# Performance work log

Measured on AMD Instinct MI355X. Metric: run time of the kernel, lower is better.

Reference implementation:

```python
import jax, jax.numpy as jnp
import numpy as np

B, N, E = 2, 2048, 1024
H = 16
NE = 16                                  # num experts
TOPN = 2
CAP = max(4, int(N * 1.25 / NE))         # expert capacity = 160 (train, cf=1.25)
HFF = int(E * 4 * 2 / 3)                 # 2730, Expert_alt hidden
EPS = 1e-9
BLOCK = 64                               # spatial block size for block-causal mask


def setup_inputs():
    key = jax.random.key(0)
    ks = jax.random.split(key, 16)
    def nrm(k, shape, s=0.02):
        return jax.random.normal(k, shape, dtype=jnp.float32) * s
    # block-causal mask (tril over time blocks, repeat_interleave spatially); True = masked
    blk = np.tril(np.ones((N // BLOCK, N // BLOCK)))
    blk = np.repeat(np.repeat(blk, BLOCK, axis=0), BLOCK, axis=1)
    attn_mask = jnp.asarray(~blk.astype(bool))
    return dict(
        x=jax.random.normal(ks[0], (B, N, E), jnp.float32),
        attn_mask=attn_mask,
        in_proj_w=nrm(ks[1], (3 * E, E)),
        in_proj_b=jnp.zeros((3 * E,), jnp.float32),
        out_proj_w=nrm(ks[2], (E, E)),
        out_proj_b=jnp.zeros((E,), jnp.float32),
        rms_gamma=jnp.ones((E,), jnp.float32),
        gate_w=nrm(ks[3], (NE, E)),
        ln_g=jnp.ones((NE, E), jnp.float32),
        ln_b=jnp.zeros((NE, E), jnp.float32),
        w1=nrm(ks[4], (NE, HFF, E)),
        b1=jnp.zeros((NE, HFF), jnp.float32),
        w2=nrm(ks[5], (NE, E, HFF)),
        b2=jnp.zeros((NE, E), jnp.float32),
        route_unif=jax.random.uniform(ks[6], (TOPN, B, N), jnp.float32),
    )


def _layernorm(t, g, b, eps=1e-5):
    mu = t.mean(-1, keepdims=True)
    var = ((t - mu) ** 2).mean(-1, keepdims=True)
    return (t - mu) * jax.lax.rsqrt(var + eps) * g + b


def _forward(x, attn_mask, in_proj_w, in_proj_b, out_proj_w, out_proj_b,
             rms_gamma, gate_w, ln_g, ln_b, w1, b1, w2, b2, route_unif):
    dh = E // H
    # ---- multi-head self-attention (torch nn.MultiheadAttention math) ----
    qkv = x @ in_proj_w.T + in_proj_b                       # (B,N,3E)
    q, k, v = jnp.split(qkv, 3, axis=-1)
    to_heads = lambda t: t.reshape(B, N, H, dh).transpose(0, 2, 1, 3)
    q, k, v = to_heads(q), to_heads(k), to_heads(v)
    scores = jnp.einsum('bhqd,bhkd->bhqk', q, k) / jnp.sqrt(jnp.float32(dh))
    scores = jnp.where(attn_mask[None, None], -jnp.inf, scores)
    attn = jax.nn.softmax(scores, axis=-1)
    o = jnp.einsum('bhqk,bhkd->bhqd', attn, v).transpose(0, 2, 1, 3).reshape(B, N, E)
    o = o @ out_proj_w.T + out_proj_b
    y = o + x                                               # residual around MHA

    # ---- SparseMoEBlock: RMSNorm prenorm -> MoE -> residual ----
    residual = y
    nrm = y / jnp.clip(jnp.linalg.norm(y, axis=-1, keepdims=True), 1e-12)
    moe_in = nrm * jnp.sqrt(jnp.float32(E)) * rms_gamma

    # ---- top-2 gating (st-moe TopNGating, training mode) ----
    logits = moe_in @ gate_w.T                              # (B,N,NE)
    raw_gates = jax.nn.softmax(logits, axis=-1)
    gates_v, gate_idx = jax.lax.top_k(raw_gates, TOPN)      # (B,N,2)
    gates = jnp.moveaxis(gates_v, -1, 0)                    # (2,B,N)
    gate_idx = jnp.moveaxis(gate_idx, -1, 0)
    one_hot_idx = jax.nn.one_hot(gate_idx, NE, dtype=jnp.float32)  # (2,B,N,NE)
    mask = one_hot_idx
    mask_1 = mask[0]
    denom = jnp.clip(gates.sum(0, keepdims=True), EPS)
    gates = gates / denom
    threshold = jnp.array([EPS, 0.2], jnp.float32)[:, None, None]
    should_route = route_unif < gates / jnp.clip(threshold, EPS)
    should_route = should_route.at[0].set(True)             # always route to top-1
    mask = mask * should_route[..., None].astype(jnp.float32)
    mask_cumsum = jnp.cumsum(mask, axis=-2) - mask          # exclusive cumsum over N

    positions, masks_k = [], []
    prev = jnp.zeros((B, 1, NE), jnp.float32)
    capf = jnp.float32(CAP)
    for n_ in range(TOPN):
        pos = (mask_cumsum[n_] + prev) * mask[n_]           # (B,N,NE)
        mk = mask[n_] * (pos < capf).astype(jnp.float32)    # drop over-capacity
        prev = prev + mk.sum(axis=-2, keepdims=True)
        positions.append(pos.sum(-1))                       # (B,N)
        masks_k.append(mk)
    positions = jnp.stack(positions)                        # (2,B,N)
    mask = jnp.stack(masks_k)
    mask_flat = mask.sum(-1)                                # (2,B,N)
    gates = gates * mask_flat

    pos_oh = jax.nn.one_hot(positions.astype(jnp.int32), CAP, dtype=jnp.float32)  # (2,B,N,CAP)
    combine = jnp.einsum('kbn,kbn,kbne,kbnc->bnec', gates, mask_flat, one_hot_idx, pos_oh)
    dispatch_hard = (combine > 0).astype(jnp.float32)
    dispatch = dispatch_hard + combine - jax.lax.stop_gradient(combine)  # straight-through

    # ---- aux losses ----
    density_1 = mask_1.mean(-2)                             # (B,NE)
    density_proxy = raw_gates.mean(-2)
    balance_loss = (density_proxy * density_1).mean() * jnp.float32(NE ** 2)
    router_z_loss = jnp.mean(jax.nn.logsumexp(logits, axis=-1) ** 2)

    # ---- dispatch -> experts -> combine ----
    expert_inputs = jnp.einsum('bnd,bnec->ebcd', moe_in, dispatch)  # (NE,B,CAP,E)

    def expert_fn(g, bl, W1, B1, W2, B2, xin):
        h = _layernorm(xin, g, bl)
        h = h @ W1.T + B1
        h = jnp.where(h >= 0, h, 0.01 * h)                  # LeakyReLU(0.01)
        return h @ W2.T + B2

    expert_out = jax.vmap(expert_fn)(ln_g, ln_b, w1, b1, w2, b2, expert_inputs)
    moe_out = jnp.einsum('bnec,ebcd->bnd', combine, expert_out)

    out = moe_out + residual
    total_aux = balance_loss * 0.01 + router_z_loss * 0.001
    return out, total_aux, balance_loss, router_z_loss


def reference(x, attn_mask, in_proj_w, in_proj_b, out_proj_w, out_proj_b,
              rms_gamma, gate_w, ln_g, ln_b, w1, b1, w2, b2, route_unif):
    return _forward(x, attn_mask, in_proj_w, in_proj_b, out_proj_w, out_proj_b,
                    rms_gamma, gate_w, ln_g, ln_b, w1, b1, w2, b2, route_unif)
```

## Files before the change

### kernel.cpp

```cpp
#include <hip/hip_runtime.h>
#include <hip/hip_bf16.h>
#include <cstdint>

#define NSEQ  2048
#define BSZ   2
#define NTOK  4096
#define EDIM  1024
#define NEXP  16
#define CAPC  160
#define HFF_R 2730
#define HFF_P 2752

typedef __bf16 bf16_t;
typedef __bf16 bf16x8 __attribute__((ext_vector_type(8)));
typedef __bf16 bf16x4 __attribute__((ext_vector_type(4)));
typedef float  f32x4  __attribute__((ext_vector_type(4)));
typedef unsigned int uint32;

__device__ inline bf16x8 zero8() {
    bf16x8 v;
#pragma unroll
    for (int i = 0; i < 8; i++) v[i] = (bf16_t)0.f;
    return v;
}
__device__ inline bf16x8 pack8(float4 a, float4 b) {
    bf16x8 v;
    v[0]=(bf16_t)a.x; v[1]=(bf16_t)a.y; v[2]=(bf16_t)a.z; v[3]=(bf16_t)a.w;
    v[4]=(bf16_t)b.x; v[5]=(bf16_t)b.y; v[6]=(bf16_t)b.z; v[7]=(bf16_t)b.w;
    return v;
}
struct hl_t { bf16_t h, l; };
__device__ inline hl_t split1(float f) {
    hl_t r;
    r.h = (bf16_t)f;
    r.l = (bf16_t)(f - (float)r.h);
    return r;
}

template <int EPI, int C_SPLIT>
__global__ __launch_bounds__(256) void gemm_split(
    const float* __restrict__ A, const float* __restrict__ Bw,
    const float* __restrict__ bias, const float* __restrict__ resid,
    bf16_t* __restrict__ Chi, bf16_t* __restrict__ Clo, float* __restrict__ Cf,
    int M, int N, int K, int scale_cut, float scale_val)
// ... 72 lines not shown
                acc[i][j] = __builtin_amdgcn_mfma_f32_16x16x32_bf16(amh[i], bnl[j], acc[i][j], 0, 0, 0);
                acc[i][j] = __builtin_amdgcn_mfma_f32_16x16x32_bf16(aml[i], bnh[j], acc[i][j], 0, 0, 0);
            }
        __builtin_amdgcn_s_setprio(0);
        __syncthreads();
    }

#pragma unroll
    for (int i = 0; i < 4; i++) {
        int mgb = m0 + wm * 64 + i * 16 + lg * 4;
#pragma unroll
        for (int j = 0; j < 4; j++) {
            int ng = n0 + wn * 64 + j * 16 + l15;
            float bval = bias[ng];
#pragma unroll
            for (int r = 0; r < 4; r++) {
                int mg = mgb + r;
                float val = acc[i][j][r] + bval;
                if (scale_cut > 0 && ng < scale_cut) val *= scale_val;
                if (EPI == 2) val += resid[(long)mg * N + ng];
                long idx = (long)mg * N + ng;
                if (C_SPLIT) {
                    bf16_t hi = (bf16_t)val;
                    Chi[idx] = hi;
                    Clo[idx] = (bf16_t)(val - (float)hi);
                } else {
                    Cf[idx] = val;
                }
            }
        }
    }
}

template <int EPI, int C_BF16>
__global__ __launch_bounds__(256) void gemm_nt64(
    const bf16_t* __restrict__ Av, const float* __restrict__ Bw,
    const float* __restrict__ bias, void* __restrict__ Cv,
    int M, int N, int Nwr, int KA, int KB,
    long sAe, long sBe, long sBiasE, long sCe, int ldc)
{
    __shared__ __align__(16) bf16_t Alds[64 * 72];
    __shared__ __align__(16) bf16_t Blds[64 * 72];
    const int t = threadIdx.x;
    const int e = blockIdx.z;
    const int m0 = blockIdx.y * 64, n0 = blockIdx.x * 64;
    const int lane = t & 63, l15 = lane & 15, lg = lane >> 4;
    const int wid = t >> 6, wm = wid >> 1, wn = wid & 1;
    const int srow = t >> 2, scol = (t & 3) * 16;

    f32x4 acc[2][2];
    const f32x4 zf = {0.f, 0.f, 0.f, 0.f};
#pragma unroll
    for (int i = 0; i < 2; i++)
#pragma unroll
        for (int j = 0; j < 2; j++) acc[i][j] = zf;

    bf16x8 sa0, sa1;
    float4 sb0, sb1, sb2, sb3;
    const float4 zf4 = {0.f, 0.f, 0.f, 0.f};
    auto LOADA = [&](int k0) {
        int mg = m0 + srow;
        sa0 = zero8(); sa1 = zero8();
        if (mg < M) {
            const bf16_t* ap = Av + (long)e * sAe + (long)mg * KA + k0 + scol;
            sa0 = *(const bf16x8*)ap;
            sa1 = *(const bf16x8*)(ap + 8);
        }
    };
    auto LOADB = [&](int k0) {
        int ng = n0 + srow;
        if (ng < N) {
            const float* bp = Bw + (long)e * sBe + (long)ng * KB + k0 + scol;
            if (k0 + 64 <= KB) {
                sb0 = *(const float4*)bp;       sb1 = *(const float4*)(bp + 4);
                sb2 = *(const float4*)(bp + 8); sb3 = *(const float4*)(bp + 12);
            } else {
                float v[16];
#pragma unroll
                for (int i = 0; i < 16; i++) {
                    int kk = k0 + scol + i;
                    v[i] = (kk < KB) ? bp[i] : 0.f;
                }
                sb0 = *(float4*)&v[0];  sb1 = *(float4*)&v[4];
                sb2 = *(float4*)&v[8];  sb3 = *(float4*)&v[12];
            }
        } else {
            sb0 = zf4; sb1 = zf4; sb2 = zf4; sb3 = zf4;
        }
    };
    auto WRITEAB = [&]() {
        *(bf16x8*)&Alds[srow * 72 + scol]     = sa0;
        *(bf16x8*)&Alds[srow * 72 + scol + 8] = sa1;
        *(bf16x8*)&Blds[srow * 72 + scol]     = pack8(sb0, sb1);
        *(bf16x8*)&Blds[srow * 72 + scol + 8] = pack8(sb2, sb3);
    };

    LOADA(0); LOADB(0);
    for (int k0 = 0; k0 < KA; k0 += 64) {
        WRITEAB();
        __syncthreads();
        if (k0 + 64 < KA) { LOADA(k0 + 64); LOADB(k0 + 64); }
#pragma unroll
        for (int ks = 0; ks < 2; ks++) {
            bf16x8 am[2], bn[2];
#pragma unroll
            for (int i = 0; i < 2; i++)
                am[i] = *(const bf16x8*)&Alds[(wm * 32 + i * 16 + l15) * 72 + ks * 32 + lg * 8];
#pragma unroll
            for (int j = 0; j < 2; j++)
                bn[j] = *(const bf16x8*)&Blds[(wn * 32 + j * 16 + l15) * 72 + ks * 32 + lg * 8];
            __builtin_amdgcn_s_setprio(1);
#pragma unroll
            for (int i = 0; i < 2; i++)
#pragma unroll
                for (int j = 0; j < 2; j++)
                    acc[i][j] = __builtin_amdgcn_mfma_f32_16x16x32_bf16(am[i], bn[j], acc[i][j], 0, 0, 0);
            __builtin_amdgcn_s_setprio(0);
        }
        __syncthreads();
    }

    const float* biasp = bias + (long)e * sBiasE;
#pragma unroll
    for (int i = 0; i < 2; i++) {
        int mgb = m0 + wm * 32 + i * 16 + lg * 4;
#pragma unroll
        for (int j = 0; j < 2; j++) {
            int ng = n0 + wn * 32 + j * 16 + l15;
            if (ng < Nwr) {
                float bval = (ng < N) ? biasp[ng] : 0.f;
#pragma unroll
                for (int r = 0; r < 4; r++) {
                    int mg = mgb + r;
                    if (mg < M) {
                        float val = acc[i][j][r] + bval;
                        if (EPI == 1) val = (val >= 0.f) ? val : 0.01f * val;
                        if (ng >= N) val = 0.f;
                        long cidx = (long)e * sCe + (long)mg * ldc + ng;
                        if (C_BF16) ((bf16_t*)Cv)[cidx] = (bf16_t)val;
                        else        ((float*)Cv)[cidx] = val;
                    }
                }
            }
        }
    }
}

__global__ __launch_bounds__(256) void attn_split(const bf16_t* __restrict__ qh,
                                                  const bf16_t* __restrict__ ql,
                                                  float* __restrict__ o)
{
    __shared__ __align__(16) bf16_t KhS[64 * 72], KlS[64 * 72];
    __shared__ __align__(16) bf16_t VhS[64 * 72], VlS[64 * 72];
    __shared__ __align__(16) bf16_t PhS[4][2][16 * 72], PlS[4][2][16 * 72];

    const int id = blockIdx.x;
    const int x  = id & 7;
    const int s  = id >> 3;
    const int b  = s >> 5;
    const int s5 = s & 31;
    const int qraw = s5 & 15;
    const int h  = x + 8 * (s5 >> 4);
    const int qt = b ? (15 - qraw) : qraw;
    const int nkb = 2 * qt + 2;

    const int t = threadIdx.x, wid = t >> 6, lane = t & 63, l15 = lane & 15, lg = lane >> 4;
    const int krow = t >> 2, kdc = (t & 3) * 16;
    const int vk = t & 63, vdg = (t >> 6) * 16;
    const long kvb = (long)(b * NSEQ) * 3072 + 1024 + h * 64;
    const f32x4 zf = {0.f, 0.f, 0.f, 0.f};

    const long qo0 = (long)(b * NSEQ + qt * 128 + wid * 16 + l15) * 3072 + h * 64 + lg * 8;
    const long qo1 = qo0 + (long)64 * 3072;
    bf16x8 q0h0 = *(const bf16x8*)(qh + qo0), q0h1 = *(const bf16x8*)(qh + qo0 + 32);
    bf16x8 q0l0 = *(const bf16x8*)(ql + qo0), q0l1 = *(const bf16x8*)(ql + qo0 + 32);
    bf16x8 q1h0 = *(const bf16x8*)(qh + qo1), q1h1 = *(const bf16x8*)(qh + qo1 + 32);
    bf16x8 q1l0 = *(const bf16x8*)(ql + qo1), q1l1 = *(const bf16x8*)(ql + qo1 + 32);

    f32x4 O0[4], O1[4];
    float m0r[4], l0r[4], m1r[4], l1r[4];
#pragma unroll
    for (int r = 0; r < 4; r++) {
        O0[r] = zf; O1[r] = zf;
        m0r[r] = -1e30f; l0r[r] = 0.f; m1r[r] = -1e30f; l1r[r] = 0.f;
    }

    bf16x8 skh0, skh1, skl0, skl1, svh0, svh1, svl0, svl1;
    auto LOADKV = [&](int kb) {
        long ko = kvb + (long)(kb * 64 + krow) * 3072 + kdc;
        skh0 = *(const bf16x8*)(qh + ko); skh1 = *(const bf16x8*)(qh + ko + 8);
        skl0 = *(const bf16x8*)(ql + ko); skl1 = *(const bf16x8*)(ql + ko + 8);
        long vo = kvb + 1024 + (long)(kb * 64 + vk) * 3072 + vdg;
        svh0 = *(const bf16x8*)(qh + vo); svh1 = *(const bf16x8*)(qh + vo + 8);
        svl0 = *(const bf16x8*)(ql + vo); svl1 = *(const bf16x8*)(ql + vo + 8);
    };
    auto WRITEKV = [&]() {
        *(bf16x8*)&KhS[krow * 72 + kdc]     = skh0;
        *(bf16x8*)&KhS[krow * 72 + kdc + 8] = skh1;
        *(bf16x8*)&KlS[krow * 72 + kdc]     = skl0;
        *(bf16x8*)&KlS[krow * 72 + kdc + 8] = skl1;
#pragma unroll
        for (int i = 0; i < 8; i++) {
            VhS[(vdg + i) * 72 + vk]     = svh0[i];
            VhS[(vdg + 8 + i) * 72 + vk] = svh1[i];
            VlS[(vdg + i) * 72 + vk]     = svl0[i];
            VlS[(vdg + 8 + i) * 72 + vk] = svl1[i];
        }
    };

    LOADKV(0);
    for (int kb = 0; kb < nkb; kb++) {
        __syncthreads();
        WRITEKV();
        __syncthreads();
        if (kb + 1 < nkb) LOADKV(kb + 1);
        const bool g0a = (kb < nkb - 1);
        f32x4 s0[4], s1[4];
        __builtin_amdgcn_s_setprio(1);
#pragma unroll
        for (int ks = 0; ks < 4; ks++) {
            int base = (ks * 16 + l15) * 72 + lg * 8;
            bf16x8 kh0 = *(const bf16x8*)&KhS[base];
            bf16x8 kh1 = *(const bf16x8*)&KhS[base + 32];
            bf16x8 kl0 = *(const bf16x8*)&KlS[base];
            bf16x8 kl1 = *(const bf16x8*)&KlS[base + 32];
            f32x4 a = zf;
            a = __builtin_amdgcn_mfma_f32_16x16x32_bf16(q1h0, kh0, a, 0, 0, 0);
            a = __builtin_amdgcn_mfma_f32_16x16x32_bf16(q1h1, kh1, a, 0, 0, 0);
            a = __builtin_amdgcn_mfma_f32_16x16x32_bf16(q1h0, kl0, a, 0, 0, 0);
            a = __builtin_amdgcn_mfma_f32_16x16x32_bf16(q1h1, kl1, a, 0, 0, 0);
            a = __builtin_amdgcn_mfma_f32_16x16x32_bf16(q1l0, kh0, a, 0, 0, 0);
            a = __builtin_amdgcn_mfma_f32_16x16x32_bf16(q1l1, kh1, a, 0, 0, 0);
            s1[ks] = a;
            f32x4 c = zf;
            if (g0a) {
                c = __builtin_amdgcn_mfma_f32_16x16x32_bf16(q0h0, kh0, c, 0, 0, 0);
                c = __builtin_amdgcn_mfma_f32_16x16x32_bf16(q0h1, kh1, c, 0, 0, 0);
                c = __builtin_amdgcn_mfma_f32_16x16x32_bf16(q0h0, kl0, c, 0, 0, 0);
                c = __builtin_amdgcn_mfma_f32_16x16x32_bf16(q0h1, kl1, c, 0, 0, 0);
                c = __builtin_amdgcn_mfma_f32_16x16x32_bf16(q0l0, kh0, c, 0, 0, 0);
                c = __builtin_amdgcn_mfma_f32_16x16x32_bf16(q0l1, kh1, c, 0, 0, 0);
            }
            s0[ks] = c;
        }
        __builtin_amdgcn_s_setprio(0);
        {
            float alpha[4];
#pragma unroll
            for (int r = 0; r < 4; r++) {
                float mt = fmaxf(fmaxf(s1[0][r], s1[1][r]), fmaxf(s1[2][r], s1[3][r]));
#pragma unroll
                for (int m = 1; m < 16; m <<= 1) mt = fmaxf(mt, __shfl_xor(mt, m));
                float mn = fmaxf(m1r[r], mt);
                alpha[r] = __expf(m1r[r] - mn);
                m1r[r] = mn;
            }
            float ladd[4] = {0.f, 0.f, 0.f, 0.f};
#pragma unroll
            for (int ks = 0; ks < 4; ks++)
#pragma unroll
                for (int r = 0; r < 4; r++) {
                    float p = __expf(s1[ks][r] - m1r[r]);
                    s1[ks][r] = p;
                    ladd[r] += p;
                }
#pragma unroll
            for (int r = 0; r < 4; r++) {
#pragma unroll
                for (int m = 1; m < 16; m <<= 1) ladd[r] += __shfl_xor(ladd[r], m);
                l1r[r] = l1r[r] * alpha[r] + ladd[r];
            }
#pragma unroll
            for (int sb = 0; sb < 4; sb++)
#pragma unroll
                for (int r = 0; r < 4; r++) O1[sb][r] *= alpha[r];
            bf16_t* pwh = &PhS[wid][1][0];
            bf16_t* pwl = &PlS[wid][1][0];
#pragma unroll
            for (int ks = 0; ks < 4; ks++)
#pragma unroll
                for (int r = 0; r < 4; r++) {
                    hl_t pv = split1(s1[ks][r]);
                    pwh[(lg * 4 + r) * 72 + ks * 16 + l15] = pv.h;
                    pwl[(lg * 4 + r) * 72 + ks * 16 + l15] = pv.l;
                }
        }
        if (g0a) {
            float alpha[4];
#pragma unroll
            for (int r = 0; r < 4; r++) {
                float mt = fmaxf(fmaxf(s0[0][r], s0[1][r]), fmaxf(s0[2][r], s0[3][r]));
#pragma unroll
                for (int m = 1; m < 16; m <<= 1) mt = fmaxf(mt, __shfl_xor(mt, m));
                float mn = fmaxf(m0r[r], mt);
                alpha[r] = __expf(m0r[r] - mn);
                m0r[r] = mn;
            }
            float ladd[4] = {0.f, 0.f, 0.f, 0.f};
#pragma unroll
            for (int ks = 0; ks < 4; ks++)
#pragma unroll
                for (int r = 0; r < 4; r++) {
                    float p = __expf(s0[ks][r] - m0r[r]);
                    s0[ks][r] = p;
                    ladd[r] += p;
                }
#pragma unroll
            for (int r = 0; r < 4; r++) {
#pragma unroll
                for (int m = 1; m < 16; m <<= 1) ladd[r] += __shfl_xor(ladd[r], m);
                l0r[r] = l0r[r] * alpha[r] + ladd[r];
            }
#pragma unroll
            for (int sb = 0; sb < 4; sb++)
#pragma unroll
                for (int r = 0; r < 4; r++) O0[sb][r] *= alpha[r];
            bf16_t* pwh = &PhS[wid][0][0];
            bf16_t* pwl = &PlS[wid][0][0];
#pragma unroll
            for (int ks = 0; ks < 4; ks++)
#pragma unroll
                for (int r = 0; r < 4; r++) {
                    hl_t pv = split1(s0[ks][r]);
                    pwh[(lg * 4 + r) * 72 + ks * 16 + l15] = pv.h;
                    pwl[(lg * 4 + r) * 72 + ks * 16 + l15] = pv.l;
                }
        }
        __builtin_amdgcn_s_setprio(1);
#pragma unroll
        for (int kst = 0; kst < 2; kst++) {
            bf16x8 pf1h = *(const bf16x8*)&PhS[wid][1][l15 * 72 + kst * 32 + lg * 8];
            bf16x8 pf1l = *(const bf16x8*)&PlS[wid][1][l15 * 72 + kst * 32 + lg * 8];
            bf16x8 pf0h, pf0l;
            if (g0a) {
                pf0h = *(const bf16x8*)&PhS[wid][0][l15 * 72 + kst * 32 + lg * 8];
                pf0l = *(const bf16x8*)&PlS[wid][0][l15 * 72 + kst * 32 + lg * 8];
            }
#pragma unroll
            for (int sb = 0; sb < 4; sb++) {
                int base = (sb * 16 + l15) * 72 + kst * 32 + lg * 8;
                bf16x8 vfh = *(const bf16x8*)&VhS[base];
                bf16x8 vfl = *(const bf16x8*)&VlS[base];
                O1[sb] = __builtin_amdgcn_mfma_f32_16x16x32_bf16(pf1h, vfh, O1[sb], 0, 0, 0);
                O1[sb] = __builtin_amdgcn_mfma_f32_16x16x32_bf16(pf1h, vfl, O1[sb], 0, 0, 0);
                O1[sb] = __builtin_amdgcn_mfma_f32_16x16x32_bf16(pf1l, vfh, O1[sb], 0, 0, 0);
                if (g0a) {
                    O0[sb] = __builtin_amdgcn_mfma_f32_16x16x32_bf16(pf0h, vfh, O0[sb], 0, 0, 0);
                    O0[sb] = __builtin_amdgcn_mfma_f32_16x16x32_bf16(pf0h, vfl, O0[sb], 0, 0, 0);
                    O0[sb] = __builtin_amdgcn_mfma_f32_16x16x32_bf16(pf0l, vfh, O0[sb], 0, 0, 0);
                }
            }
        }
        __builtin_amdgcn_s_setprio(0);
    }
#pragma unroll
    for (int sb = 0; sb < 4; sb++)
#pragma unroll
        for (int r = 0; r < 4; r++) {
            int qg0 = qt * 128 + wid * 16 + lg * 4 + r;
            int col = h * 64 + sb * 16 + l15;
            o[(long)(b * NSEQ + qg0) * 1024 + col] = O0[sb][r] / l0r[r];
            o[(long)(b * NSEQ + qg0 + 64) * 1024 + col] = O1[sb][r] / l1r[r];
        }
}

__global__ __launch_bounds__(256) void rmsnorm_kernel(const float* __restrict__ y,
                                                      const float* __restrict__ gamma,
                                                      float* __restrict__ moe)
{
    long base = (long)blockIdx.x * 1024;
    float4 v = ((const float4*)(y + base))[threadIdx.x];
    float ss = v.x * v.x + v.y * v.y + v.z * v.z + v.w * v.w;
#pragma unroll
    for (int m = 32; m; m >>= 1) ss += __shfl_xor(ss, m);
    __shared__ float ls[4];
    if ((threadIdx.x & 63) == 0) ls[threadIdx.x >> 6] = ss;
    __syncthreads();
    float tot = ls[0] + ls[1] + ls[2] + ls[3];
    float sc = 32.0f / fmaxf(sqrtf(tot), 1e-12f);
    float4 g = ((const float4*)gamma)[threadIdx.x];
    float4 ov;
    ov.x = v.x * sc * g.x; ov.y = v.y * sc * g.y; ov.z = v.z * sc * g.z; ov.w = v.w * sc * g.w;
    ((float4*)(moe + base))[threadIdx.x] = ov;
}

__global__ __launch_bounds__(256) void gating_kernel(
    const float* __restrict__ moe, const float* __restrict__ gw,
    const float* __restrict__ runif, uint32* __restrict__ tokpack,
    float* __restrict__ tokg, float* __restrict__ acc)
{
    const int wid = threadIdx.x >> 6, lane = threadIdx.x & 63;
    const int tk = blockIdx.x * 4 + wid;
    const int b = tk >> 11, n = tk & 2047;
    float xv[16];
    const float4* xr4 = (const float4*)(moe + (long)tk * 1024 + lane * 16);
#pragma unroll
// ... 246 lines not shown
    const float* out_w = (const float*)d_in[4];
    const float* out_b = (const float*)d_in[5];
    const float* rg    = (const float*)d_in[6];
    const float* gw    = (const float*)d_in[7];
    const float* lng   = (const float*)d_in[8];
    const float* lnb   = (const float*)d_in[9];
    const float* w1    = (const float*)d_in[10];
    const float* b1    = (const float*)d_in[11];
    const float* w2    = (const float*)d_in[12];
    const float* b2    = (const float*)d_in[13];
    const float* runif = (const float*)d_in[14];
    float* out = (float*)d_out;

    size_t off = 0;
    char* wsb = (char*)d_ws;
    auto take = [&](size_t bytes) -> char* {
        char* p = wsb + off;
        off += (bytes + 255) & ~(size_t)255;
        return p;
    };
    bf16_t* qkvh = (bf16_t*)take((size_t)NTOK * 3072 * 2);
    bf16_t* qkvl = (bf16_t*)take((size_t)NTOK * 3072 * 2);
    float*  obuf = (float*)take((size_t)NTOK * 1024 * 4);
    float*  ybuf = (float*)take((size_t)NTOK * 1024 * 4);
    float*  moe  = (float*)take((size_t)NTOK * 1024 * 4);
    bf16_t* eln  = (bf16_t*)take((size_t)NEXP * BSZ * CAPC * 1024 * 2);
    bf16_t* hbuf = (bf16_t*)take((size_t)NEXP * BSZ * CAPC * HFF_P * 2);
    uint32* tokpack = (uint32*)take(NTOK * 4);
    float*  tokg = (float*)take(NTOK * 8);
    uint32* r0   = (uint32*)take(NTOK * 4);
    uint32* r1   = (uint32*)take(NTOK * 4);
    int*    prev = (int*)take(128);
    float*  acc  = (float*)take(1024);
    float*  ein  = (float*)qkvl;
    float*  eoutv = (float*)qkvh;

    zero_acc_kernel<<<1, 128, 0, stream>>>(acc);

    gemm_split<0, 1><<<dim3(24, 32), 256, 0, stream>>>(
        x, in_w, in_b, nullptr, qkvh, qkvl, nullptr,
        NTOK, 3072, 1024, 1024, 0.125f);

    attn_split<<<dim3(512), 256, 0, stream>>>(qkvh, qkvl, obuf);

    gemm_split<2, 0><<<dim3(8, 32), 256, 0, stream>>>(
        obuf, out_w, out_b, x, nullptr, nullptr, ybuf,
        NTOK, 1024, 1024, 0, 1.0f);

    rmsnorm_kernel<<<NTOK, 256, 0, stream>>>(ybuf, rg, moe);
    gating_kernel<<<NTOK / 4, 256, 0, stream>>>(moe, gw, runif, tokpack, tokg, acc);
    scan_kernel<<<dim3(BSZ), 512, 0, stream>>>(tokpack, r0, r1, prev);
    gather_kernel<<<NTOK, 256, 0, stream>>>(moe, r0, r1, prev, ein);
    expert_ln_kernel<<<NEXP * BSZ * CAPC, 256, 0, stream>>>(ein, lng, lnb, eln);

    gemm_nt64<1, 1><<<dim3(43, 5, 16), 256, 0, stream>>>(
        eln, w1, b1, hbuf, 320, HFF_R, HFF_P, 1024, 1024,
        (long)320 * 1024, (long)HFF_R * 1024, HFF_R, (long)320 * HFF_P, HFF_P);

    gemm_nt64<0, 0><<<dim3(16, 5, 16), 256, 0, stream>>>(
        hbuf, w2, b2, eoutv, 320, 1024, 1024, HFF_P, HFF_R,
        (long)320 * HFF_P, (long)1024 * HFF_R, 1024, (long)320 * 1024, 1024);

    combine_kernel<<<NTOK, 256, 0, stream>>>(ybuf, eoutv, r0, r1, tokg, prev, out);
    finalize_kernel<<<1, 64, 0, stream>>>(acc, out + (size_t)NTOK * 1024);
}
```

Baseline: 687.9 us.

## Split attention KV range across blocks with merge kernel; widen expert GEMM1 tiles

Attention now gives each block one short and one long query tile (pairing pr with 15-pr), and splits the KV range of each into two halves handled by separate blocks. Each block writes unnormalized partial outputs plus per-row max and sum, and a new merge kernel combines the two halves with log-sum-exp weights. The aim is to even out causal load imbalance across blocks. Separately, the first expert GEMM switches to a new 64x128 tile kernel with K step 32, which halves the grid in N and increases reuse of each A tile. The cost is extra fp32 partial-output traffic, an added launch for the merge, and reuse of the eln buffer as scratch.

```diff
diff --git a/kernel.cpp b/kernel.cpp
--- a/kernel.cpp
+++ b/kernel.cpp
@@ -10,6 +10,7 @@
 #define CAPC  160
 #define HFF_R 2730
 #define HFF_P 2752
+#define OTOT  4194304
 
 typedef __bf16 bf16_t;
 typedef __bf16 bf16x8 __attribute__((ext_vector_type(8)));
@@ -148,6 +149,121 @@
     }
 }
 
+template <int EPI, int C_BF16, int BM>
+__global__ __launch_bounds__(256) void gemm_ntA(
+    const bf16_t* __restrict__ Av, const float* __restrict__ Bw,
+    const float* __restrict__ bias, void* __restrict__ Cv,
+    int M, int N, int Nwr, int KA, int KB,
+    long sAe, long sBe, long sBiasE, long sCe, int ldc)
+{
+    constexpr int MI = BM / 32;
+    __shared__ __align__(16) bf16_t Alds[BM * 40];
+    __shared__ __align__(16) bf16_t Blds[128 * 40];
+    const int t = threadIdx.x;
+    const int e = blockIdx.z;
+    const int m0 = blockIdx.y * BM, n0 = blockIdx.x * 128;
+    const int lane = t & 63, l15 = lane & 15, lg = lane >> 4;
+    const int wid = t >> 6, wm = wid >> 1, wn = wid & 1;
+    const int arow = (BM == 128) ? (t >> 1) : (t >> 2);
+    const int acol = (BM == 128) ? ((t & 1) * 16) : ((t & 3) * 8);
+    const int brow = t >> 1, bcol = (t & 1) * 16;
+
+    f32x4 acc[MI][4];
+    const f32x4 zf = {0.f, 0.f, 0.f, 0.f};
+#pragma unroll
+    for (int i = 0; i < MI; i++)
+#pragma unroll
+        for (int j = 0; j < 4; j++) acc[i][j] = zf;
+
+    bf16x8 sa0, sa1;
+    float4 sb0, sb1, sb2, sb3;
+    const float4 zf4 = {0.f, 0.f, 0.f, 0.f};
+    auto LOADA = [&](int k0) {
+        int mg = m0 + arow;
+        sa0 = zero8();
+        if (BM == 128) sa1 = zero8();
+        if (mg < M) {
+            const bf16_t* ap = Av + (long)e * sAe + (long)mg * KA + k0 + acol;
+            sa0 = *(const bf16x8*)ap;
+            if (BM == 128) sa1 = *(const bf16x8*)(ap + 8);
+        }
+    };
+    auto LOADB = [&](int k0) {
+        int ng = n0 + brow;
+        if (ng < N) {
+            const float* bp = Bw + (long)e * sBe + (long)ng * KB + k0 + bcol;
+            if (k0 + 32 <= KB) {
+                sb0 = *(const float4*)bp;       sb1 = *(const float4*)(bp + 4);
+                sb2 = *(const float4*)(bp + 8); sb3 = *(const float4*)(bp + 12);
+            } else {
+                float v[16];
+#pragma unroll
+                for (int i = 0; i < 16; i++) {
+                    int kk = k0 + bcol + i;
+                    v[i] = (kk < KB) ? bp[i] : 0.f;
+                }
+                sb0 = *(float4*)&v[0];  sb1 = *(float4*)&v[4];
+                sb2 = *(float4*)&v[8];  sb3 = *(float4*)&v[12];
+            }
+        } else {
+            sb0 = zf4; sb1 = zf4; sb2 = zf4; sb3 = zf4;
+        }
+    };
+    auto WRITEAB = [&]() {
+        *(bf16x8*)&Alds[arow * 40 + acol] = sa0;
+        if (BM == 128) *(bf16x8*)&Alds[arow * 40 + acol + 8] = sa1;
+        *(bf16x8*)&Blds[brow * 40 + bcol] = pack8(sb0, sb1);
+        *(bf16x8*)&Blds[brow * 40 + bcol + 8] = pack8(sb2, sb3);
+    };
+
+    LOADA(0); LOADB(0);
+    for (int k0 = 0; k0 < KA; k0 += 32) {
+        WRITEAB();
+        __syncthreads();
+        if (k0 + 32 < KA) { LOADA(k0 + 32); LOADB(k0 + 32); }
+        bf16x8 am[MI], bn[4];
+#pragma unroll
+        for (int i = 0; i < MI; i++)
+            am[i] = *(const bf16x8*)&Alds[(wm * (BM / 2) + i * 16 + l15) * 40 + lg * 8];
+#pragma unroll
+        for (int j = 0; j < 4; j++)
+            bn[j] = *(const bf16x8*)&Blds[(wn * 64 + j * 16 + l15) * 40 + lg * 8];
+        __builtin_amdgcn_s_setprio(1);
+#pragma unroll
+        for (int i = 0; i < MI; i++)
+#pragma unroll
+            for (int j = 0; j < 4; j++)
+                acc[i][j] = __builtin_amdgcn_mfma_f32_16x16x32_bf16(am[i], bn[j], acc[i][j], 0, 0, 0);
+        __builtin_amdgcn_s_setprio(0);
+        __syncthreads();
+    }
+
+    const float* biasp = bias + (long)e * sBiasE;
+#pragma unroll
+    for (int i = 0; i < MI; i++) {
+        int mgb = m0 + wm * (BM / 2) + i * 16 + lg * 4;
+#pragma unroll
+        for (int j = 0; j < 4; j++) {
+            int ng = n0 + wn * 64 + j * 16 + l15;
+            if (ng < Nwr) {
+                float bval = (ng < N) ? biasp[ng] : 0.f;
+#pragma unroll
+                for (int r = 0; r < 4; r++) {
+                    int mg = mgb + r;
+                    if (mg < M) {
+                        float val = acc[i][j][r] + bval;
+                        if (EPI == 1) val = (val >= 0.f) ? val : 0.01f * val;
+                        if (ng >= N) val = 0.f;
+                        long cidx = (long)e * sCe + (long)mg * ldc + ng;
+                        if (C_BF16) ((bf16_t*)Cv)[cidx] = (bf16_t)val;
+                        else        ((float*)Cv)[cidx] = val;
+                    }
+                }
+            }
+        }
+    }
+}
+
 template <int EPI, int C_BF16>
 __global__ __launch_bounds__(256) void gemm_nt64(
     const bf16_t* __restrict__ Av, const float* __restrict__ Bw,
@@ -264,7 +380,8 @@
 
 __global__ __launch_bounds__(256) void attn_split(const bf16_t* __restrict__ qh,
                                                   const bf16_t* __restrict__ ql,
-                                                  float* __restrict__ o)
+                                                  float* __restrict__ opart,
+                                                  float* __restrict__ ml)
 {
     __shared__ __align__(16) bf16_t KhS[64 * 72], KlS[64 * 72];
     __shared__ __align__(16) bf16_t VhS[64 * 72], VlS[64 * 72];
@@ -273,33 +390,17 @@
     const int id = blockIdx.x;
     const int x  = id & 7;
     const int s  = id >> 3;
-    const int b  = s >> 5;
-    const int s5 = s & 31;
-    const int qraw = s5 & 15;
-    const int h  = x + 8 * (s5 >> 4);
-    const int qt = b ? (15 - qraw) : qraw;
-    const int nkb = 2 * qt + 2;
+    const int pr = s & 7;
+    const int hg = (s >> 3) & 1;
+    const int b  = (s >> 4) & 1;
+    const int half = s >> 5;
+    const int h  = x + 8 * hg;
 
     const int t = threadIdx.x, wid = t >> 6, lane = t & 63, l15 = lane & 15, lg = lane >> 4;
     const int krow = t >> 2, kdc = (t & 3) * 16;
     const int vk = t & 63, vdg = (t >> 6) * 16;
     const long kvb = (long)(b * NSEQ) * 3072 + 1024 + h * 64;
     const f32x4 zf = {0.f, 0.f, 0.f, 0.f};
-
-    const long qo0 = (long)(b * NSEQ + qt * 128 + wid * 16 + l15) * 3072 + h * 64 + lg * 8;
-    const long qo1 = qo0 + (long)64 * 3072;
-    bf16x8 q0h0 = *(const bf16x8*)(qh + qo0), q0h1 = *(const bf16x8*)(qh + qo0 + 32);
-    bf16x8 q0l0 = *(const bf16x8*)(ql + qo0), q0l1 = *(const bf16x8*)(ql + qo0 + 32);
-    bf16x8 q1h0 = *(const bf16x8*)(qh + qo1), q1h1 = *(const bf16x8*)(qh + qo1 + 32);
-    bf16x8 q1l0 = *(const bf16x8*)(ql + qo1), q1l1 = *(const bf16x8*)(ql + qo1 + 32);
-
-    f32x4 O0[4], O1[4];
-    float m0r[4], l0r[4], m1r[4], l1r[4];
-#pragma unroll
-    for (int r = 0; r < 4; r++) {
-        O0[r] = zf; O1[r] = zf;
-        m0r[r] = -1e30f; l0r[r] = 0.f; m1r[r] = -1e30f; l1r[r] = 0.f;
-    }
 
     bf16x8 skh0, skh1, skl0, skl1, svh0, svh1, svl0, svl1;
     auto LOADKV = [&](int kb) {
@@ -324,160 +425,217 @@
         }
     };
 
-    LOADKV(0);
-    for (int kb = 0; kb < nkb; kb++) {
-        __syncthreads();
-        WRITEKV();
-        __syncthreads();
-        if (kb + 1 < nkb) LOADKV(kb + 1);
-        const bool g0a = (kb < nkb - 1);
-        f32x4 s0[4], s1[4];
-        __builtin_amdgcn_s_setprio(1);
-#pragma unroll
-        for (int ks = 0; ks < 4; ks++) {
-            int base = (ks * 16 + l15) * 72 + lg * 8;
-            bf16x8 kh0 = *(const bf16x8*)&KhS[base];
-            bf16x8 kh1 = *(const bf16x8*)&KhS[base + 32];
-            bf16x8 kl0 = *(const bf16x8*)&KlS[base];
-            bf16x8 kl1 = *(const bf16x8*)&KlS[base + 32];
-            f32x4 a = zf;
-            a = __builtin_amdgcn_mfma_f32_16x16x32_bf16(q1h0, kh0, a, 0, 0, 0);
-            a = __builtin_amdgcn_mfma_f32_16x16x32_bf16(q1h1, kh1, a, 0, 0, 0);
-            a = __builtin_amdgcn_mfma_f32_16x16x32_bf16(q1h0, kl0, a, 0, 0, 0);
-            a = __builtin_amdgcn_mfma_f32_16x16x32_bf16(q1h1, kl1, a, 0, 0, 0);
-            a = __builtin_amdgcn_mfma_f32_16x16x32_bf16(q1l0, kh0, a, 0, 0, 0);
-            a = __builtin_amdgcn_mfma_f32_16x16x32_bf16(q1l1, kh1, a, 0, 0, 0);
-            s1[ks] = a;
-            f32x4 c = zf;
+    for (int seg = 0; seg < 2; seg++) {
+        const int qt = seg ? (15 - pr) : pr;
+        const int nkb = 2 * qt + 2;
+        const int hs = qt + 1;
+        const int kb0 = half * hs, kb1 = kb0 + hs;
+
+        const long qo0 = (long)(b * NSEQ + qt * 128 + wid * 16 + l15) * 3072 + h * 64 + lg * 8;
+        const long qo1 = qo0 + (long)64 * 3072;
+        bf16x8 q0h0 = *(const bf16x8*)(qh + qo0), q0h1 = *(const bf16x8*)(qh + qo0 + 32);
+        bf16x8 q0l0 = *(const bf16x8*)(ql + qo0), q0l1 = *(const bf16x8*)(ql + qo0 + 32);
+        bf16x8 q1h0 = *(const bf16x8*)(qh + qo1), q1h1 = *(const bf16x8*)(qh + qo1 + 32);
+        bf16x8 q1l0 = *(const bf16x8*)(ql + qo1), q1l1 = *(const bf16x8*)(ql + qo1 + 32);
+
+        f32x4 O0[4], O1[4];
+        float m0r[4], l0r[4], m1r[4], l1r[4];
+#pragma unroll
+        for (int r = 0; r < 4; r++) {
+            O0[r] = zf; O1[r] = zf;
+            m0r[r] = -1e30f; l0r[r] = 0.f; m1r[r] = -1e30f; l1r[r] = 0.f;
+        }
+
+        LOADKV(kb0);
+        for (int kb = kb0; kb < kb1; kb++) {
+            __syncthreads();
+            WRITEKV();
+            __syncthreads();
+            if (kb + 1 < kb1) LOADKV(kb + 1);
+            const bool g0a = (kb < nkb - 1);
+            f32x4 s0[4], s1[4];
+            __builtin_amdgcn_s_setprio(1);
+#pragma unroll
+            for (int ks = 0; ks < 4; ks++) {
+                int base = (ks * 16 + l15) * 72 + lg * 8;
+                bf16x8 kh0 = *(const bf16x8*)&KhS[base];
+                bf16x8 kh1 = *(const bf16x8*)&KhS[base + 32];
+                bf16x8 kl0 = *(const bf16x8*)&KlS[base];
+                bf16x8 kl1 = *(const bf16x8*)&KlS[base + 32];
+                f32x4 a = zf;
+                a = __builtin_amdgcn_mfma_f32_16x16x32_bf16(q1h0, kh0, a, 0, 0, 0);
+                a = __builtin_amdgcn_mfma_f32_16x16x32_bf16(q1h1, kh1, a, 0, 0, 0);
+                a = __builtin_amdgcn_mfma_f32_16x16x32_bf16(q1h0, kl0, a, 0, 0, 0);
+                a = __builtin_amdgcn_mfma_f32_16x16x32_bf16(q1h1, kl1, a, 0, 0, 0);
+                a = __builtin_amdgcn_mfma_f32_16x16x32_bf16(q1l0, kh0, a, 0, 0, 0);
+                a = __builtin_amdgcn_mfma_f32_16x16x32_bf16(q1l1, kh1, a, 0, 0, 0);
+                s1[ks] = a;
+                f32x4 c = zf;
+                if (g0a) {
+                    c = __builtin_amdgcn_mfma_f32_16x16x32_bf16(q0h0, kh0, c, 0, 0, 0);
+                    c = __builtin_amdgcn_mfma_f32_16x16x32_bf16(q0h1, kh1, c, 0, 0, 0);
+                    c = __builtin_amdgcn_mfma_f32_16x16x32_bf16(q0h0, kl0, c, 0, 0, 0);
+                    c = __builtin_amdgcn_mfma_f32_16x16x32_bf16(q0h1, kl1, c, 0, 0, 0);
+                    c = __builtin_amdgcn_mfma_f32_16x16x32_bf16(q0l0, kh0, c, 0, 0, 0);
+                    c = __builtin_amdgcn_mfma_f32_16x16x32_bf16(q0l1, kh1, c, 0, 0, 0);
+                }
+                s0[ks] = c;
+            }
+            __builtin_amdgcn_s_setprio(0);
+            {
+                float alpha[4];
+#pragma unroll
+                for (int r = 0; r < 4; r++) {
+                    float mt = fmaxf(fmaxf(s1[0][r], s1[1][r]), fmaxf(s1[2][r], s1[3][r]));
+#pragma unroll
+                    for (int m = 1; m < 16; m <<= 1) mt = fmaxf(mt, __shfl_xor(mt, m));
+                    float mn = fmaxf(m1r[r], mt);
+                    alpha[r] = __expf(m1r[r] - mn);
+                    m1r[r] = mn;
+                }
+                float ladd[4] = {0.f, 0.f, 0.f, 0.f};
+#pragma unroll
+                for (int ks = 0; ks < 4; ks++)
+#pragma unroll
+                    for (int r = 0; r < 4; r++) {
+                        float p = __expf(s1[ks][r] - m1r[r]);
+                        s1[ks][r] = p;
+                        ladd[r] += p;
+                    }
+#pragma unroll
+                for (int r = 0; r < 4; r++) {
+#pragma unroll
+                    for (int m = 1; m < 16; m <<= 1) ladd[r] += __shfl_xor(ladd[r], m);
+                    l1r[r] = l1r[r] * alpha[r] + ladd[r];
+                }
+#pragma unroll
+                for (int sb = 0; sb < 4; sb++)
+#pragma unroll
+                    for (int r = 0; r < 4; r++) O1[sb][r] *= alpha[r];
+                bf16_t* pwh = &PhS[wid][1][0];
+                bf16_t* pwl = &PlS[wid][1][0];
+#pragma unroll
+                for (int ks = 0; ks < 4; ks++)
+#pragma unroll
+                    for (int r = 0; r < 4; r++) {
+                        hl_t pv = split1(s1[ks][r]);
+                        pwh[(lg * 4 + r) * 72 + ks * 16 + l15] = pv.h;
+                        pwl[(lg * 4 + r) * 72 + ks * 16 + l15] = pv.l;
+                    }
+            }
             if (g0a) {
-                c = __builtin_amdgcn_mfma_f32_16x16x32_bf16(q0h0, kh0, c, 0, 0, 0);
-                c = __builtin_amdgcn_mfma_f32_16x16x32_bf16(q0h1, kh1, c, 0, 0, 0);
-                c = __builtin_amdgcn_mfma_f32_16x16x32_bf16(q0h0, kl0, c, 0, 0, 0);
-                c = __builtin_amdgcn_mfma_f32_16x16x32_bf16(q0h1, kl1, c, 0, 0, 0);
-                c = __builtin_amdgcn_mfma_f32_16x16x32_bf16(q0l0, kh0, c, 0, 0, 0);
-                c = __builtin_amdgcn_mfma_f32_16x16x32_bf16(q0l1, kh1, c, 0, 0, 0);
-            }
-            s0[ks] = c;
-        }
-        __builtin_amdgcn_s_setprio(0);
-        {
-            float alpha[4];
+                float alpha[4];
+#pragma unroll
+                for (int r = 0; r < 4; r++) {
+                    float mt = fmaxf(fmaxf(s0[0][r], s0[1][r]), fmaxf(s0[2][r], s0[3][r]));
+#pragma unroll
+                    for (int m = 1; m < 16; m <<= 1) mt = fmaxf(mt, __shfl_xor(mt, m));
+                    float mn = fmaxf(m0r[r], mt);
+                    alpha[r] = __expf(m0r[r] - mn);
+                    m0r[r] = mn;
+                }
+                float ladd[4] = {0.f, 0.f, 0.f, 0.f};
+#pragma unroll
+                for (int ks = 0; ks < 4; ks++)
+#pragma unroll
+                    for (int r = 0; r < 4; r++) {
+                        float p = __expf(s0[ks][r] - m0r[r]);
+                        s0[ks][r] = p;
+                        ladd[r] += p;
+                    }
+#pragma unroll
+                for (int r = 0; r < 4; r++) {
+#pragma unroll
+                    for (int m = 1; m < 16; m <<= 1) ladd[r] += __shfl_xor(ladd[r], m);
+                    l0r[r] = l0r[r] * alpha[r] + ladd[r];
+                }
+#pragma unroll
+                for (int sb = 0; sb < 4; sb++)
+#pragma unroll
+                    for (int r = 0; r < 4; r++) O0[sb][r] *= alpha[r];
+                bf16_t* pwh = &PhS[wid][0][0];
+                bf16_t* pwl = &PlS[wid][0][0];
+#pragma unroll
+                for (int ks = 0; ks < 4; ks++)
+#pragma unroll
+                    for (int r = 0; r < 4; r++) {
+                        hl_t pv = split1(s0[ks][r]);
+                        pwh[(lg * 4 + r) * 72 + ks * 16 + l15] = pv.h;
+                        pwl[(lg * 4 + r) * 72 + ks * 16 + l15] = pv.l;
+                    }
+            }
+            __builtin_amdgcn_s_setprio(1);
+#pragma unroll
+            for (int kst = 0; kst < 2; kst++) {
+                bf16x8 pf1h = *(const bf16x8*)&PhS[wid][1][l15 * 72 + kst * 32 + lg * 8];
+                bf16x8 pf1l = *(const bf16x8*)&PlS[wid][1][l15 * 72 + kst * 32 + lg * 8];
+                bf16x8 pf0h, pf0l;
+                if (g0a) {
+                    pf0h = *(const bf16x8*)&PhS[wid][0][l15 * 72 + kst * 32 + lg * 8];
+                    pf0l = *(const bf16x8*)&PlS[wid][0][l15 * 72 + kst * 32 + lg * 8];
+                }
+#pragma unroll
+                for (int sb = 0; sb < 4; sb++) {
+                    int base = (sb * 16 + l15) * 72 + kst * 32 + lg * 8;
+                    bf16x8 vfh = *(const bf16x8*)&VhS[base];
+                    bf16x8 vfl = *(const bf16x8*)&VlS[base];
+                    O1[sb] = __builtin_amdgcn_mfma_f32_16x16x32_bf16(pf1h, vfh, O1[sb], 0, 0, 0);
+                    O1[sb] = __builtin_amdgcn_mfma_f32_16x16x32_bf16(pf1h, vfl, O1[sb], 0, 0, 0);
+                    O1[sb] = __builtin_amdgcn_mfma_f32_16x16x32_bf16(pf1l, vfh, O1[sb], 0, 0, 0);
+                    if (g0a) {
+                        O0[sb] = __builtin_amdgcn_mfma_f32_16x16x32_bf16(pf0h, vfh, O0[sb], 0, 0, 0);
+                        O0[sb] = __builtin_amdgcn_mfma_f32_16x16x32_bf16(pf0h, vfl, O0[sb], 0, 0, 0);
+                        O0[sb] = __builtin_amdgcn_mfma_f32_16x16x32_bf16(pf0l, vfh, O0[sb], 0, 0, 0);
+                    }
+                }
+            }
+            __builtin_amdgcn_s_setprio(0);
+        }
+        float* op = opart + (size_t)half * OTOT;
+#pragma unroll
+        for (int sb = 0; sb < 4; sb++)
 #pragma unroll
             for (int r = 0; r < 4; r++) {
-                float mt = fmaxf(fmaxf(s1[0][r], s1[1][r]), fmaxf(s1[2][r], s1[3][r]));
-#pragma unroll
-                for (int m = 1; m < 16; m <<= 1) mt = fmaxf(mt, __shfl_xor(mt, m));
-                float mn = fmaxf(m1r[r], mt);
-                alpha[r] = __expf(m1r[r] - mn);
-                m1r[r] = mn;
-            }
-            float ladd[4] = {0.f, 0.f, 0.f, 0.f};
-#pragma unroll
-            for (int ks = 0; ks < 4; ks++)
-#pragma unroll
-                for (int r = 0; r < 4; r++) {
-                    float p = __expf(s1[ks][r] - m1r[r]);
-                    s1[ks][r] = p;
-                    ladd[r] += p;
-                }
+                int qg0 = qt * 128 + wid * 16 + lg * 4 + r;
+                int col = h * 64 + sb * 16 + l15;
+                op[(long)(b * NSEQ + qg0) * 1024 + col] = O0[sb][r];
+                op[(long)(b * NSEQ + qg0 + 64) * 1024 + col] = O1[sb][r];
+            }
+        if (l15 == 0) {
 #pragma unroll
             for (int r = 0; r < 4; r++) {
-#pragma unroll
-                for (int m = 1; m < 16; m <<= 1) ladd[r] += __shfl_xor(ladd[r], m);
-                l1r[r] = l1r[r] * alpha[r] + ladd[r];
-            }
-#pragma unroll
-            for (int sb = 0; sb < 4; sb++)
-#pragma unroll
-                for (int r = 0; r < 4; r++) O1[sb][r] *= alpha[r];
-            bf16_t* pwh = &PhS[wid][1][0];
-            bf16_t* pwl = &PlS[wid][1][0];
-#pragma unroll
-            for (int ks = 0; ks < 4; ks++)
-#pragma unroll
-                for (int r = 0; r < 4; r++) {
-                    hl_t pv = split1(s1[ks][r]);
-                    pwh[(lg * 4 + r) * 72 + ks * 16 + l15] = pv.h;
-                    pwl[(lg * 4 + r) * 72 + ks * 16 + l15] = pv.l;
-                }
-        }
-        if (g0a) {
-            float alpha[4];
-#pragma unroll
-            for (int r = 0; r < 4; r++) {
-                float mt = fmaxf(fmaxf(s0[0][r], s0[1][r]), fmaxf(s0[2][r], s0[3][r]));
-#pragma unroll
-                for (int m = 1; m < 16; m <<= 1) mt = fmaxf(mt, __shfl_xor(mt, m));
-                float mn = fmaxf(m0r[r], mt);
-                alpha[r] = __expf(m0r[r] - mn);
-                m0r[r] = mn;
-            }
-            float ladd[4] = {0.f, 0.f, 0.f, 0.f};
-#pragma unroll
-            for (int ks = 0; ks < 4; ks++)
-#pragma unroll
-                for (int r = 0; r < 4; r++) {
-                    float p = __expf(s0[ks][r] - m0r[r]);
-                    s0[ks][r] = p;
-                    ladd[r] += p;
-                }
-#pragma unroll
-            for (int r = 0; r < 4; r++) {
-#pragma unroll
-                for (int m = 1; m < 16; m <<= 1) ladd[r] += __shfl_xor(ladd[r], m);
-                l0r[r] = l0r[r] * alpha[r] + ladd[r];
-            }
-#pragma unroll
-            for (int sb = 0; sb < 4; sb++)
-#pragma unroll
-                for (int r = 0; r < 4; r++) O0[sb][r] *= alpha[r];
-            bf16_t* pwh = &PhS[wid][0][0];
-            bf16_t* pwl = &PlS[wid][0][0];
-#pragma unroll
-            for (int ks = 0; ks < 4; ks++)
-#pragma unroll
-                for (int r = 0; r < 4; r++) {
-                    hl_t pv = split1(s0[ks][r]);
-                    pwh[(lg * 4 + r) * 72 + ks * 16 + l15] = pv.h;
-                    pwl[(lg * 4 + r) * 72 + ks * 16 + l15] = pv.l;
-                }
-        }
-        __builtin_amdgcn_s_setprio(1);
-#pragma unroll
-        for (int kst = 0; kst < 2; kst++) {
-            bf16x8 pf1h = *(const bf16x8*)&PhS[wid][1][l15 * 72 + kst * 32 + lg * 8];
-            bf16x8 pf1l = *(const bf16x8*)&PlS[wid][1][l15 * 72 + kst * 32 + lg * 8];
-            bf16x8 pf0h, pf0l;
-            if (g0a) {
-                pf0h = *(const bf16x8*)&PhS[wid][0][l15 * 72 + kst * 32 + lg * 8];
-                pf0l = *(const bf16x8*)&PlS[wid][0][l15 * 72 + kst * 32 + lg * 8];
-            }
-#pragma unroll
-            for (int sb = 0; sb < 4; sb++) {
-                int base = (sb * 16 + l15) * 72 + kst * 32 + lg * 8;
-                bf16x8 vfh = *(const bf16x8*)&VhS[base];
-                bf16x8 vfl = *(const bf16x8*)&VlS[base];
-                O1[sb] = __builtin_amdgcn_mfma_f32_16x16x32_bf16(pf1h, vfh, O1[sb], 0, 0, 0);
-                O1[sb] = __builtin_amdgcn_mfma_f32_16x16x32_bf16(pf1h, vfl, O1[sb], 0, 0, 0);
-                O1[sb] = __builtin_amdgcn_mfma_f32_16x16x32_bf16(pf1l, vfh, O1[sb], 0, 0, 0);
-                if (g0a) {
-                    O0[sb] = __builtin_amdgcn_mfma_f32_16x16x32_bf16(pf0h, vfh, O0[sb], 0, 0, 0);
-                    O0[sb] = __builtin_amdgcn_mfma_f32_16x16x32_bf16(pf0h, vfl, O0[sb], 0, 0, 0);
-                    O0[sb] = __builtin_amdgcn_mfma_f32_16x16x32_bf16(pf0l, vfh, O0[sb], 0, 0, 0);
-                }
-            }
-        }
-        __builtin_amdgcn_s_setprio(0);
-    }
-#pragma unroll
-    for (int sb = 0; sb < 4; sb++)
-#pragma unroll
-        for (int r = 0; r < 4; r++) {
-            int qg0 = qt * 128 + wid * 16 + lg * 4 + r;
-            int col = h * 64 + sb * 16 + l15;
-            o[(long)(b * NSEQ + qg0) * 1024 + col] = O0[sb][r] / l0r[r];
-            o[(long)(b * NSEQ + qg0 + 64) * 1024 + col] = O1[sb][r] / l1r[r];
-        }
+                int qg0 = qt * 128 + wid * 16 + lg * 4 + r;
+                long i0 = ((long)(half * 2 + b) * 2048 + qg0) * 32 + h * 2;
+                long i1 = ((long)(half * 2 + b) * 2048 + qg0 + 64) * 32 + h * 2;
+                ml[i0] = m0r[r]; ml[i0 + 1] = l0r[r];
+                ml[i1] = m1r[r]; ml[i1 + 1] = l1r[r];
+            }
+        }
+    }
+}
+
+__global__ __launch_bounds__(256) void merge_attn(const float* __restrict__ opart,
+                                                  const float* __restrict__ ml,
+                                                  float* __restrict__ o)
+{
+    const int tok = blockIdx.x, i = threadIdx.x;
+    const int h = i >> 4;
+    const int b = tok >> 11, qrow = tok & 2047;
+    long i0 = ((long)(0 * 2 + b) * 2048 + qrow) * 32 + h * 2;
+    long i1 = ((long)(1 * 2 + b) * 2048 + qrow) * 32 + h * 2;
+    float m0 = ml[i0], l0 = ml[i0 + 1];
+    float m1 = ml[i1], l1 = ml[i1 + 1];
+    float m = fmaxf(m0, m1);
+    float w0 = __expf(m0 - m), w1 = __expf(m1 - m);
+    float inv = 1.f / (l0 * w0 + l1 * w1);
+    float4 o0 = ((const float4*)(opart + (long)tok * 1024))[i];
+    float4 o1 = ((const float4*)(opart + OTOT + (long)tok * 1024))[i];
+    float4 ov;
+    ov.x = (o0.x * w0 + o1.x * w1) * inv;
+    ov.y = (o0.y * w0 + o1.y * w1) * inv;
+    ov.z = (o0.z * w0 + o1.z * w1) * inv;
+    ov.w = (o0.w * w0 + o1.w * w1) * inv;
+    ((float4*)(o + (long)tok * 1024))[i] = ov;
 }
 
 __global__ __launch_bounds__(256) void rmsnorm_kernel(const float* __restrict__ y,
@@ -790,8 +948,10 @@
     uint32* r1   = (uint32*)take(NTOK * 4);
     int*    prev = (int*)take(128);
     float*  acc  = (float*)take(1024);
-    float*  ein  = (float*)qkvl;
+    float*  ein   = (float*)qkvl;
     float*  eoutv = (float*)qkvh;
+    float*  opart = (float*)eln;
+    float*  mlbuf = opart + 2 * (size_t)OTOT;
 
     zero_acc_kernel<<<1, 128, 0, stream>>>(acc);
 
@@ -799,7 +959,8 @@
         x, in_w, in_b, nullptr, qkvh, qkvl, nullptr,
         NTOK, 3072, 1024, 1024, 0.125f);
 
-    attn_split<<<dim3(512), 256, 0, stream>>>(qkvh, qkvl, obuf);
+    attn_split<<<dim3(512), 256, 0, stream>>>(qkvh, qkvl, opart, mlbuf);
+    merge_attn<<<dim3(NTOK), 256, 0, stream>>>(opart, mlbuf, obuf);
 
     gemm_split<2, 0><<<dim3(8, 32), 256, 0, stream>>>(
         obuf, out_w, out_b, x, nullptr, nullptr, ybuf,
@@ -811,7 +972,7 @@
     gather_kernel<<<NTOK, 256, 0, stream>>>(moe, r0, r1, prev, ein);
     expert_ln_kernel<<<NEXP * BSZ * CAPC, 256, 0, stream>>>(ein, lng, lnb, eln);
 
-    gemm_nt64<1, 1><<<dim3(43, 5, 16), 256, 0, stream>>>(
+    gemm_ntA<1, 1, 64><<<dim3(22, 5, 16), 256, 0, stream>>>(
         eln, w1, b1, hbuf, 320, HFF_R, HFF_P, 1024, 1024,
         (long)320 * 1024, (long)HFF_R * 1024, HFF_R, (long)320 * HFF_P, HFF_P);
 
```

Measured after the change: 698.6 us. Within noise of the previous version (+1.6%).

## Cover all 320 expert rows per block so each fp32 weight tile loads once

Applied to the files above, without the earlier changes.

The expert FFN GEMMs now give each block the full 320-row M dimension of one expert and a 64-column N tile, instead of 64x64 tiles spread over a 3D grid. Each fp32 weight tile is then read from global memory and converted to bf16 once, not five times. The cost is fewer blocks (688 and 256), much higher register use (20 accumulators plus 10 staged A vectors per thread) and a larger LDS footprint. Together these lower occupancy and may hurt latency hiding.

```diff
diff --git a/kernel.cpp b/kernel.cpp
--- a/kernel.cpp
+++ b/kernel.cpp
@@ -149,38 +149,39 @@
 }
 
 template <int EPI, int C_BF16>
-__global__ __launch_bounds__(256) void gemm_nt64(
+__global__ __launch_bounds__(256) void gemm_ffn(
     const bf16_t* __restrict__ Av, const float* __restrict__ Bw,
     const float* __restrict__ bias, void* __restrict__ Cv,
-    int M, int N, int Nwr, int KA, int KB,
+    int N, int Nwr, int KA, int KB,
     long sAe, long sBe, long sBiasE, long sCe, int ldc)
 {
-    __shared__ __align__(16) bf16_t Alds[64 * 72];
+    __shared__ __align__(16) bf16_t Alds[320 * 72];
     __shared__ __align__(16) bf16_t Blds[64 * 72];
+    const int id = blockIdx.x;
+    const int e = id & 15, nt = id >> 4;
+    const int n0 = nt * 64;
     const int t = threadIdx.x;
-    const int e = blockIdx.z;
-    const int m0 = blockIdx.y * 64, n0 = blockIdx.x * 64;
     const int lane = t & 63, l15 = lane & 15, lg = lane >> 4;
     const int wid = t >> 6, wm = wid >> 1, wn = wid & 1;
     const int srow = t >> 2, scol = (t & 3) * 16;
 
-    f32x4 acc[2][2];
+    f32x4 acc[10][2];
     const f32x4 zf = {0.f, 0.f, 0.f, 0.f};
 #pragma unroll
-    for (int i = 0; i < 2; i++)
+    for (int i = 0; i < 10; i++)
 #pragma unroll
         for (int j = 0; j < 2; j++) acc[i][j] = zf;
 
-    bf16x8 sa0, sa1;
+    bf16x8 sa[5][2];
     float4 sb0, sb1, sb2, sb3;
     const float4 zf4 = {0.f, 0.f, 0.f, 0.f};
     auto LOADA = [&](int k0) {
-        int mg = m0 + srow;
-        sa0 = zero8(); sa1 = zero8();
-        if (mg < M) {
-            const bf16_t* ap = Av + (long)e * sAe + (long)mg * KA + k0 + scol;
-            sa0 = *(const bf16x8*)ap;
-            sa1 = *(const bf16x8*)(ap + 8);
+        const bf16_t* abase = Av + (long)e * sAe + k0 + scol;
+#pragma unroll
+        for (int p = 0; p < 5; p++) {
+            const bf16_t* ap = abase + (long)(srow + 64 * p) * KA;
+            sa[p][0] = *(const bf16x8*)ap;
+            sa[p][1] = *(const bf16x8*)(ap + 8);
         }
     };
     auto LOADB = [&](int k0) {
@@ -205,8 +206,11 @@
         }
     };
     auto WRITEAB = [&]() {
-        *(bf16x8*)&Alds[srow * 72 + scol]     = sa0;
-        *(bf16x8*)&Alds[srow * 72 + scol + 8] = sa1;
+#pragma unroll
+        for (int p = 0; p < 5; p++) {
+            *(bf16x8*)&Alds[(srow + 64 * p) * 72 + scol]     = sa[p][0];
+            *(bf16x8*)&Alds[(srow + 64 * p) * 72 + scol + 8] = sa[p][1];
+        }
         *(bf16x8*)&Blds[srow * 72 + scol]     = pack8(sb0, sb1);
         *(bf16x8*)&Blds[srow * 72 + scol + 8] = pack8(sb2, sb3);
     };
@@ -218,16 +222,17 @@
         if (k0 + 64 < KA) { LOADA(k0 + 64); LOADB(k0 + 64); }
 #pragma unroll
         for (int ks = 0; ks < 2; ks++) {
-            bf16x8 am[2], bn[2];
-#pragma unroll
-            for (int i = 0; i < 2; i++)
-                am[i] = *(const bf16x8*)&Alds[(wm * 32 + i * 16 + l15) * 72 + ks * 32 + lg * 8];
+            bf16x8 bn[2];
 #pragma unroll
             for (int j = 0; j < 2; j++)
                 bn[j] = *(const bf16x8*)&Blds[(wn * 32 + j * 16 + l15) * 72 + ks * 32 + lg * 8];
+            bf16x8 am[10];
+#pragma unroll
+            for (int i = 0; i < 10; i++)
+                am[i] = *(const bf16x8*)&Alds[(wm * 160 + i * 16 + l15) * 72 + ks * 32 + lg * 8];
             __builtin_amdgcn_s_setprio(1);
 #pragma unroll
-            for (int i = 0; i < 2; i++)
+            for (int i = 0; i < 10; i++)
 #pragma unroll
                 for (int j = 0; j < 2; j++)
                     acc[i][j] = __builtin_amdgcn_mfma_f32_16x16x32_bf16(am[i], bn[j], acc[i][j], 0, 0, 0);
@@ -238,8 +243,8 @@
 
     const float* biasp = bias + (long)e * sBiasE;
 #pragma unroll
-    for (int i = 0; i < 2; i++) {
-        int mgb = m0 + wm * 32 + i * 16 + lg * 4;
+    for (int i = 0; i < 10; i++) {
+        int mgb = wm * 160 + i * 16 + lg * 4;
 #pragma unroll
         for (int j = 0; j < 2; j++) {
             int ng = n0 + wn * 32 + j * 16 + l15;
@@ -248,14 +253,12 @@
 #pragma unroll
                 for (int r = 0; r < 4; r++) {
                     int mg = mgb + r;
-                    if (mg < M) {
-                        float val = acc[i][j][r] + bval;
-                        if (EPI == 1) val = (val >= 0.f) ? val : 0.01f * val;
-                        if (ng >= N) val = 0.f;
-                        long cidx = (long)e * sCe + (long)mg * ldc + ng;
-                        if (C_BF16) ((bf16_t*)Cv)[cidx] = (bf16_t)val;
-                        else        ((float*)Cv)[cidx] = val;
-                    }
+                    float val = acc[i][j][r] + bval;
+                    if (EPI == 1) val = (val >= 0.f) ? val : 0.01f * val;
+                    if (ng >= N) val = 0.f;
+                    long cidx = (long)e * sCe + (long)mg * ldc + ng;
+                    if (C_BF16) ((bf16_t*)Cv)[cidx] = (bf16_t)val;
+                    else        ((float*)Cv)[cidx] = val;
                 }
             }
         }
@@ -811,12 +814,12 @@
     gather_kernel<<<NTOK, 256, 0, stream>>>(moe, r0, r1, prev, ein);
     expert_ln_kernel<<<NEXP * BSZ * CAPC, 256, 0, stream>>>(ein, lng, lnb, eln);
 
-    gemm_nt64<1, 1><<<dim3(43, 5, 16), 256, 0, stream>>>(
-        eln, w1, b1, hbuf, 320, HFF_R, HFF_P, 1024, 1024,
+    gemm_ffn<1, 1><<<dim3(43 * 16), 256, 0, stream>>>(
+        eln, w1, b1, hbuf, HFF_R, HFF_P, 1024, 1024,
         (long)320 * 1024, (long)HFF_R * 1024, HFF_R, (long)320 * HFF_P, HFF_P);
 
-    gemm_nt64<0, 0><<<dim3(16, 5, 16), 256, 0, stream>>>(
-        hbuf, w2, b2, eoutv, 320, 1024, 1024, HFF_P, HFF_R,
+    gemm_ffn<0, 0><<<dim3(16 * 16), 256, 0, stream>>>(
+        hbuf, w2, b2, eoutv, 1024, 1024, HFF_P, HFF_R,
         (long)320 * HFF_P, (long)1024 * HFF_R, 1024, (long)320 * 1024, 1024);
 
     combine_kernel<<<NTOK, 256, 0, stream>>>(ybuf, eoutv, r0, r1, tokg, prev, out);
```

Measured after the change: 617.6 us. 1.11x faster.
